# Kernel optimization log

Measured on AMD Instinct MI355X. Metric: run time of the kernel, lower is better.

The kernel has to match this reference:

```python
import jax, jax.numpy as jnp
import numpy as np
from jax import lax

B, T_ENC, T_DEC, F = 64, 1024, 256, 8
U = 256          # enc_units == dec_units
H, D = 8, 32     # num_heads * key_dim == U (residual constraint)
EPS = 1e-5


def layer_norm(x, g, b):
    m = jnp.mean(x, axis=-1, keepdims=True)
    v = jnp.mean(jnp.square(x - m), axis=-1, keepdims=True)
    return g * (x - m) / jnp.sqrt(v + EPS) + b


def lstm_scan(x, W, Urec, bias, h0, c0):
    # x: [B,T,F]; keras gate order i,f,g,o
    def step(carry, xt):
        h, c = carry
        z = xt @ W + h @ Urec + bias
        i, f, g, o = jnp.split(z, 4, axis=-1)
        c = jax.nn.sigmoid(f) * c + jax.nn.sigmoid(i) * jnp.tanh(g)
        h = jax.nn.sigmoid(o) * jnp.tanh(c)
        return (h, c), h
    (h, c), hs = lax.scan(step, (h0, c0), jnp.swapaxes(x, 0, 1))
    return jnp.swapaxes(hs, 0, 1), h, c


def mha(q_in, kv_in, Wq, bq, Wk, bk, Wv, bv, Wo, bo):
    Bq, Tq = q_in.shape[0], q_in.shape[1]
    Tk = kv_in.shape[1]
    q = (q_in @ Wq + bq).reshape(Bq, Tq, H, D).transpose(0, 2, 1, 3)
    k = (kv_in @ Wk + bk).reshape(Bq, Tk, H, D).transpose(0, 2, 1, 3)
    v = (kv_in @ Wv + bv).reshape(Bq, Tk, H, D).transpose(0, 2, 1, 3)
    scores = jnp.einsum('bhqd,bhkd->bhqk', q, k) * (D ** -0.5)
    w = jax.nn.softmax(scores, axis=-1)
    ctx = jnp.einsum('bhqk,bhkd->bhqd', w, v)
    ctx = ctx.transpose(0, 2, 1, 3).reshape(Bq, Tq, H * D)
    return ctx @ Wo + bo


def setup_inputs() -> dict:
    key = jax.random.key(0)
    ks = jax.random.split(key, 24)
    g = lambda k, s: (jax.random.normal(k, s, dtype=jnp.float32) * 0.05)
    return {
        'enc_in': jax.random.normal(ks[0], (B, T_ENC, F), dtype=jnp.float32),
        'dec_in': jax.random.normal(ks[1], (B, T_DEC, F), dtype=jnp.float32),
        'ln_enc_g': jnp.ones((F,), jnp.float32), 'ln_enc_b': jnp.zeros((F,), jnp.float32),
        'W_enc': g(ks[2], (F, 4 * U)), 'U_enc': g(ks[3], (U, 4 * U)), 'b_enc': jnp.zeros((4 * U,), jnp.float32),
        'W_dec': g(ks[4], (F, 4 * U)), 'U_dec': g(ks[5], (U, 4 * U)), 'b_dec': jnp.zeros((4 * U,), jnp.float32),
        'Wq': g(ks[6], (U, H * D)), 'bq': jnp.zeros((H * D,), jnp.float32),
        'Wk': g(ks[7], (U, H * D)), 'bk': jnp.zeros((H * D,), jnp.float32),
        'Wv': g(ks[8], (U, H * D)), 'bv': jnp.zeros((H * D,), jnp.float32),
        'Wo': g(ks[9], (H * D, H * D)), 'bo': jnp.zeros((H * D,), jnp.float32),
        'ln_post_g': jnp.ones((U,), jnp.float32), 'ln_post_b': jnp.zeros((U,), jnp.float32),
        'W_out': g(ks[10], (U, 1)), 'b_out': jnp.zeros((1,), jnp.float32),
    }


def reference(enc_in, dec_in, ln_enc_g, ln_enc_b, W_enc, U_enc, b_enc,
              W_dec, U_dec, b_dec, Wq, bq, Wk, bk, Wv, bv, Wo, bo,
              ln_post_g, ln_post_b, W_out, b_out):
    x = layer_norm(enc_in, ln_enc_g, ln_enc_b)
    h0 = jnp.zeros((enc_in.shape[0], U), enc_in.dtype)
    c0 = jnp.zeros((enc_in.shape[0], U), enc_in.dtype)
    enc_seq, h, c = lstm_scan(x, W_enc, U_enc, b_enc, h0, c0)
    dec_seq, _, _ = lstm_scan(dec_in, W_dec, U_dec, b_dec, h, c)
    ctx = mha(dec_seq, enc_seq, Wq, bq, Wk, bk, Wv, bv, Wo, bo)
    mix = layer_norm(dec_seq + ctx, ln_post_g, ln_post_b)
    return mix @ W_out + b_out
```

## Files before the change

kernel.cpp:

```cpp
#include <hip/hip_runtime.h>
#include <stdint.h>

#define NBATCH 64
#define TENC   1024
#define TDEC   256
#define FDIM   8
#define UDIM   256
#define GDIM   1024
#define NHEAD  8
#define DHEAD  32
#define LNEPS  1e-5f

#define KQ 33
#define KV 27
#define KL 6

typedef unsigned int   u32;
typedef unsigned short u16;

typedef _Float16 half2v __attribute__((ext_vector_type(2)));

__device__ __forceinline__ float bf2f_lo(u32 w) { return __uint_as_float(w << 16); }
__device__ __forceinline__ float bf2f_hi(u32 w) { return __uint_as_float(w & 0xFFFF0000u); }
__device__ __forceinline__ u16 f2bf(float f) {
  u32 u = __float_as_uint(f);
  u = (u + 0x7FFFu + ((u >> 16) & 1u)) >> 16;
  return (u16)u;
}
__device__ __forceinline__ u16 f2h_bits(float f) {
  _Float16 h = (_Float16)f;
  return __builtin_bit_cast(u16, h);
}
__device__ __forceinline__ float fdot2p(u32 wp, u32 hp, float acc) {
  return __builtin_amdgcn_fdot2(__builtin_bit_cast(half2v, wp),
                                __builtin_bit_cast(half2v, hp), acc, false);
}
__device__ __forceinline__ float sigf(float x) { return 1.0f / (1.0f + __expf(-x)); }
__device__ __forceinline__ float tanhf_fast(float x) {
  float ax = fabsf(x);
  float e  = __expf(2.0f * ax);
  float r  = 1.0f - 2.0f / (e + 1.0f);
  return copysignf(r, x);
}

__global__ __launch_bounds__(256)
void k_ln8(const float* __restrict__ x, const float* __restrict__ g,
           const float* __restrict__ bt, float* __restrict__ y, int rows) {
  int r = blockIdx.x * blockDim.x + threadIdx.x;
  if (r >= rows) return;
  const float* xp = x + (size_t)r * 8;
  float4 a = ((const float4*)xp)[0];
  float4 b4 = ((const float4*)xp)[1];
  float v[8] = {a.x, a.y, a.z, a.w, b4.x, b4.y, b4.z, b4.w};
  float m = 0.f;
#pragma unroll
  for (int i = 0; i < 8; ++i) m += v[i];
  m *= 0.125f;
  float var = 0.f;
#pragma unroll
  for (int i = 0; i < 8; ++i) { float d = v[i] - m; var += d * d; }
  var *= 0.125f;
  float rs = rsqrtf(var + LNEPS);
  float o[8];
#pragma unroll
  for (int i = 0; i < 8; ++i) o[i] = g[i] * (v[i] - m) * rs + bt[i];
  float* yp = y + (size_t)r * 8;
  ((float4*)yp)[0] = make_float4(o[0], o[1], o[2], o[3]);
  ((float4*)yp)[1] = make_float4(o[4], o[5], o[6], o[7]);
}

__global__ __launch_bounds__(256)
void k_packUW3(const float* __restrict__ U, const float* __restrict__ W,
               uint4* __restrict__ out) {
  int idx = blockIdx.x * 256 + threadIdx.x;
  if (idx >= KQ * GDIM) return;
  int q = idx >> 10, col = idx & 1023;
  uint4 o;
  u32* oc = (u32*)&o;
#pragma unroll
  for (int c = 0; c < 4; ++c) {
    int p = 4 * q + c;
    int r0 = 2 * p, r1 = 2 * p + 1;
    float f0 = (r0 < 256) ? U[(size_t)r0 * GDIM + col] : W[(size_t)(r0 - 256) * GDIM + col];
    float f1 = (r1 < 256) ? U[(size_t)r1 * GDIM + col] : W[(size_t)(r1 - 256) * GDIM + col];
    oc[c] = (u32)f2h_bits(f0) | ((u32)f2h_bits(f1) << 16);
  }
  out[idx] = o;
}

__global__
__attribute__((amdgpu_flat_work_group_size(512, 512), amdgpu_waves_per_eu(2, 2)))
void k_scan8(const float* __restrict__ xseq,
             const uint4* __restrict__ Wpk,
             const float* __restrict__ bias,
             const float* __restrict__ h0, const float* __restrict__ c0,
             float* __restrict__ seq_out,
             float* __restrict__ hT, float* __restrict__ cT, int T) {
  __shared__ __align__(16) uint4 wlA[KL * 512];
  __shared__ __align__(16) uint4 wlB[KL * 512];
  __shared__ __align__(16) u32   hpk[136];
  __shared__ float zl[1024];

  const int tid = threadIdx.x, b = blockIdx.x;
  const int colA = tid, colB = tid + 512;
  u16* hpk16 = (u16*)hpk;

  uint4 wvA[KV], wvB[KV];
#pragma unroll
  for (int q = 0; q < KV; ++q) {
    wvA[q] = Wpk[(q << 10) + colA];
    asm volatile("" : "+v"(wvA[q].x), "+v"(wvA[q].y), "+v"(wvA[q].z), "+v"(wvA[q].w));
    wvB[q] = Wpk[(q << 10) + colB];
    asm volatile("" : "+v"(wvB[q].x), "+v"(wvB[q].y), "+v"(wvB[q].z), "+v"(wvB[q].w));
  }
#pragma unroll
  for (int q = 0; q < KL; ++q) {
    wlA[q * 512 + tid] = Wpk[((KV + q) << 10) + colA];
    wlB[q * 512 + tid] = Wpk[((KV + q) << 10) + colB];
  }
  const float bA = bias[colA], bB = bias[colB];

  float c_reg = 0.f, h_last = 0.f;
  if (tid < 256) {
    float hv = h0 ? h0[b * 256 + tid] : 0.f;
    c_reg = c0 ? c0[b * 256 + tid] : 0.f;
    h_last = hv;
    hpk16[tid] = f2h_bits(hv);
  }
  if (tid >= 256 && tid < 264) {
    float xv = xseq[(size_t)(b * T) * 8 + (tid - 256)];
    hpk16[tid] = f2h_bits(xv);
  }
  __syncthreads();

  for (int t = 0; t < T; ++t) {
    float xn = 0.f;
    if (tid >= 256 && tid < 264) {
      int t2 = (t + 1 < T) ? (t + 1) : (T - 1);
      xn = xseq[(size_t)(b * T + t2) * 8 + (tid - 256)];
    }
    float a0 = bA, a1 = 0.f, a2 = 0.f, a3 = 0.f;
    float b0 = bB, b1 = 0.f, b2 = 0.f, b3 = 0.f;
    const uint4* hq4 = (const uint4*)hpk;
#pragma unroll
    for (int q = 0; q < KV; ++q) {
      uint4 hh = hq4[q];
      a0 = fdot2p(wvA[q].x, hh.x, a0); a1 = fdot2p(wvA[q].y, hh.y, a1);
      a2 = fdot2p(wvA[q].z, hh.z, a2); a3 = fdot2p(wvA[q].w, hh.w, a3);
      b0 = fdot2p(wvB[q].x, hh.x, b0); b1 = fdot2p(wvB[q].y, hh.y, b1);
      b2 = fdot2p(wvB[q].z, hh.z, b2); b3 = fdot2p(wvB[q].w, hh.w, b3);
    }
#pragma unroll
    for (int q = 0; q < KL; ++q) {
      uint4 hh = hq4[KV + q];
      uint4 wA = wlA[q * 512 + tid];
      uint4 wB = wlB[q * 512 + tid];
      a0 = fdot2p(wA.x, hh.x, a0); a1 = fdot2p(wA.y, hh.y, a1);
      a2 = fdot2p(wA.z, hh.z, a2); a3 = fdot2p(wA.w, hh.w, a3);
      b0 = fdot2p(wB.x, hh.x, b0); b1 = fdot2p(wB.y, hh.y, b1);
      b2 = fdot2p(wB.z, hh.z, b2); b3 = fdot2p(wB.w, hh.w, b3);
    }
    zl[colA] = (a0 + a1) + (a2 + a3);
    zl[colB] = (b0 + b1) + (b2 + b3);
    __syncthreads();

    if (tid < 256) {
      float zi = zl[tid], zf = zl[256 + tid], zg = zl[512 + tid], zo = zl[768 + tid];
      float ig = sigf(zi), fg = sigf(zf);
      float gg = tanhf_fast(zg), og = sigf(zo);
      c_reg = fg * c_reg + ig * gg;
      float h = og * tanhf_fast(c_reg);
      h_last = h;
      seq_out[(size_t)(b * T + t) * 256 + tid] = h;
      hpk16[tid] = f2h_bits(h);
    }
    if (tid >= 256 && tid < 264) hpk16[tid] = f2h_bits(xn);
    __syncthreads();
  }
  if (hT && tid < 256) {
    hT[b * 256 + tid] = h_last;
    cT[b * 256 + tid] = c_reg;
  }
}

template <int OMODE>
__global__ __launch_bounds__(256)
void k_gemm256(const float* __restrict__ A, const float* __restrict__ Bw,
               const float* __restrict__ bias, void* __restrict__ outp,
               int M, int Tdim) {
  __shared__ __align__(16) float As[16][68];
  __shared__ __align__(16) float Bs[16][68];
  const int tid = threadIdx.x;
  const int tx = tid & 15, ty = tid >> 4;
  const int bm = blockIdx.x * 64, bn = blockIdx.y * 64;
  const int ar = tid >> 2, ac = (tid & 3) << 2;
  const int br = tid >> 4, bc = (tid & 15) << 2;
  float acc[4][4] = {};
  for (int k0 = 0; k0 < 256; k0 += 16) {
    float4 av = *(const float4*)(A + (size_t)(bm + ar) * 256 + k0 + ac);
    As[ac + 0][ar] = av.x; As[ac + 1][ar] = av.y;
    As[ac + 2][ar] = av.z; As[ac + 3][ar] = av.w;
    float4 bv = *(const float4*)(Bw + (size_t)(k0 + br) * 256 + bn + bc);
    *(float4*)&Bs[br][bc] = bv;
    __syncthreads();
#pragma unroll
    for (int k = 0; k < 16; ++k) {
      float4 a4 = *(const float4*)&As[k][ty << 2];
      float4 b4 = *(const float4*)&Bs[k][tx << 2];
      float aa[4] = {a4.x, a4.y, a4.z, a4.w};
      float bb[4] = {b4.x, b4.y, b4.z, b4.w};
#pragma unroll
      for (int i = 0; i < 4; ++i)
#pragma unroll
        for (int jj = 0; jj < 4; ++jj)
          acc[i][jj] = fmaf(aa[i], bb[jj], acc[i][jj]);
    }
    __syncthreads();
  }
#pragma unroll
  for (int i = 0; i < 4; ++i) {
    int mm = bm + (ty << 2) + i;
#pragma unroll
    for (int jj = 0; jj < 4; ++jj) {
      int n = bn + (tx << 2) + jj;
      float v = acc[i][jj] + bias[n];
      if (OMODE == 0) {
        ((float*)outp)[(size_t)mm * 256 + n] = v;
      } else {
        int bb_ = mm / Tdim, t = mm % Tdim;
        int hh = n >> 5, dd = n & 31;
        size_t o = ((((size_t)bb_ * NHEAD + hh) * Tdim) + t) * 32 + dd;
        if (OMODE == 1) ((float*)outp)[o] = v;
        else            ((u16*)outp)[o]   = f2bf(v);
      }
    }
  }
}

__global__ __launch_bounds__(256)
void k_attn(const float* __restrict__ Q, const u16* __restrict__ Kb,
            const u16* __restrict__ Vb, float* __restrict__ ctx) {
  const int bh = blockIdx.x;
  const int b = bh >> 3, h = bh & 7;
  const int tid = threadIdx.x;
  __shared__ __align__(16) float Kl[64][36];
  __shared__ __align__(16) float Vl[64][36];
  float q[32];
  {
    const float* qp = Q + ((size_t)bh * TDEC + tid) * 32;
#pragma unroll
    for (int i = 0; i < 8; ++i) {
      float4 v = ((const float4*)qp)[i];
      q[i * 4 + 0] = v.x * 0.17677669529663687f;
      q[i * 4 + 1] = v.y * 0.17677669529663687f;
      q[i * 4 + 2] = v.z * 0.17677669529663687f;
      q[i * 4 + 3] = v.w * 0.17677669529663687f;
    }
  }
  float mrun = -3.0e38f, lrun = 0.f;
  float acc[32];
#pragma unroll
  for (int i = 0; i < 32; ++i) acc[i] = 0.f;
  const int lr = tid >> 2, lc = (tid & 3) << 3;
  for (int kt = 0; kt < TENC; kt += 64) {
    {
      uint4 kw = *(const uint4*)(Kb + ((size_t)bh * TENC + kt + lr) * 32 + lc);
      Kl[lr][lc + 0] = bf2f_lo(kw.x); Kl[lr][lc + 1] = bf2f_hi(kw.x);
      Kl[lr][lc + 2] = bf2f_lo(kw.y); Kl[lr][lc + 3] = bf2f_hi(kw.y);
      Kl[lr][lc + 4] = bf2f_lo(kw.z); Kl[lr][lc + 5] = bf2f_hi(kw.z);
      Kl[lr][lc + 6] = bf2f_lo(kw.w); Kl[lr][lc + 7] = bf2f_hi(kw.w);
      uint4 vw = *(const uint4*)(Vb + ((size_t)bh * TENC + kt + lr) * 32 + lc);
      Vl[lr][lc + 0] = bf2f_lo(vw.x); Vl[lr][lc + 1] = bf2f_hi(vw.x);
      Vl[lr][lc + 2] = bf2f_lo(vw.y); Vl[lr][lc + 3] = bf2f_hi(vw.y);
      Vl[lr][lc + 4] = bf2f_lo(vw.z); Vl[lr][lc + 5] = bf2f_hi(vw.z);
      Vl[lr][lc + 6] = bf2f_lo(vw.w); Vl[lr][lc + 7] = bf2f_hi(vw.w);
    }
    __syncthreads();
#pragma unroll
    for (int cch = 0; cch < 8; ++cch) {
      float s8[8];
#pragma unroll
      for (int i = 0; i < 8; ++i) {
        const float4* kr = (const float4*)&Kl[cch * 8 + i][0];
        float ss = 0.f;
#pragma unroll
        for (int d4 = 0; d4 < 8; ++d4) {
          float4 kv = kr[d4];
          ss = fmaf(q[d4 * 4 + 0], kv.x, ss);
          ss = fmaf(q[d4 * 4 + 1], kv.y, ss);
          ss = fmaf(q[d4 * 4 + 2], kv.z, ss);
          ss = fmaf(q[d4 * 4 + 3], kv.w, ss);
        }
        s8[i] = ss;
      }
      float mnew = mrun;
#pragma unroll
      for (int i = 0; i < 8; ++i) mnew = fmaxf(mnew, s8[i]);
      float sc = __expf(mrun - mnew);
      mrun = mnew;
      lrun *= sc;
#pragma unroll
      for (int d = 0; d < 32; ++d) acc[d] *= sc;
#pragma unroll
      for (int i = 0; i < 8; ++i) {
        float p = __expf(s8[i] - mnew);
        lrun += p;
        const float4* vr = (const float4*)&Vl[cch * 8 + i][0];
#pragma unroll
        for (int d4 = 0; d4 < 8; ++d4) {
          float4 vv = vr[d4];
          acc[d4 * 4 + 0] = fmaf(p, vv.x, acc[d4 * 4 + 0]);
          acc[d4 * 4 + 1] = fmaf(p, vv.y, acc[d4 * 4 + 1]);
          acc[d4 * 4 + 2] = fmaf(p, vv.z, acc[d4 * 4 + 2]);
          acc[d4 * 4 + 3] = fmaf(p, vv.w, acc[d4 * 4 + 3]);
        }
      }
    }
    __syncthreads();
  }
  float inv = 1.0f / lrun;
  float* op = ctx + ((size_t)(b * TDEC + tid) * 256 + h * 32);
#pragma unroll
  for (int i = 0; i < 8; ++i) {
    ((float4*)op)[i] = make_float4(acc[i * 4 + 0] * inv, acc[i * 4 + 1] * inv,
                                   acc[i * 4 + 2] * inv, acc[i * 4 + 3] * inv);
  }
}

__global__ __launch_bounds__(256)
void k_final(const float* __restrict__ dec_seq, const float* __restrict__ ctxo,
             const float* __restrict__ g, const float* __restrict__ bb,
             const float* __restrict__ Wout, const float* __restrict__ bout,
             float* __restrict__ out) {
  const int wv = threadIdx.x >> 6, lane = threadIdx.x & 63;
  const int row = blockIdx.x * 4 + wv;
  const size_t base = (size_t)row * 256 + lane * 4;
  float4 dv = *(const float4*)(dec_seq + base);
  float4 cv = *(const float4*)(ctxo + base);
  float v[4] = {dv.x + cv.x, dv.y + cv.y, dv.z + cv.z, dv.w + cv.w};
  float s = v[0] + v[1] + v[2] + v[3];
#pragma unroll
  for (int off = 32; off >= 1; off >>= 1) s += __shfl_xor(s, off, 64);
  float m = s * (1.0f / 256.0f);
  float d2 = 0.f;
#pragma unroll
  for (int i = 0; i < 4; ++i) { float d = v[i] - m; d2 += d * d; }
#pragma unroll
  for (int off = 32; off >= 1; off >>= 1) d2 += __shfl_xor(d2, off, 64);
  float rs = rsqrtf(d2 * (1.0f / 256.0f) + LNEPS);
  float4 g4 = *(const float4*)(g + lane * 4);
  float4 b4 = *(const float4*)(bb + lane * 4);
  float4 w4 = *(const float4*)(Wout + lane * 4);
  float mix0 = g4.x * (v[0] - m) * rs + b4.x;
  float mix1 = g4.y * (v[1] - m) * rs + b4.y;
  float mix2 = g4.z * (v[2] - m) * rs + b4.z;
  float mix3 = g4.w * (v[3] - m) * rs + b4.w;
  float p = mix0 * w4.x + mix1 * w4.y + mix2 * w4.z + mix3 * w4.w;
#pragma unroll
  for (int off = 32; off >= 1; off >>= 1) p += __shfl_xor(p, off, 64);
  if (lane == 0) out[row] = p + bout[0];
}

extern "C" void kernel_launch(void* const* d_in, const int* in_sizes, int n_in,
                              void* d_out, int out_size, void* d_ws, size_t ws_size,
                              hipStream_t stream) {
  const float* enc_in   = (const float*)d_in[0];
  const float* dec_in   = (const float*)d_in[1];
  const float* ln_enc_g = (const float*)d_in[2];
  const float* ln_enc_b = (const float*)d_in[3];
  const float* W_enc    = (const float*)d_in[4];
  const float* U_enc    = (const float*)d_in[5];
  const float* b_enc    = (const float*)d_in[6];
  const float* W_dec    = (const float*)d_in[7];
  const float* U_dec    = (const float*)d_in[8];
  const float* b_dec    = (const float*)d_in[9];
  const float* Wq = (const float*)d_in[10]; const float* bq = (const float*)d_in[11];
  const float* Wk = (const float*)d_in[12]; const float* bk = (const float*)d_in[13];
  const float* Wv = (const float*)d_in[14]; const float* bv = (const float*)d_in[15];
  const float* Wo = (const float*)d_in[16]; const float* bo = (const float*)d_in[17];
  const float* ln_post_g = (const float*)d_in[18];
  const float* ln_post_b = (const float*)d_in[19];
  const float* W_out     = (const float*)d_in[20];
  const float* b_out     = (const float*)d_in[21];

  char* ws = (char*)d_ws;
  size_t off = 0;
  auto alloc = [&](size_t bytes) -> void* {
    void* p = ws + off;
    off += (bytes + 255) & ~(size_t)255;
    return p;
  };
  float* xln     = (float*)alloc((size_t)NBATCH * TENC * 8 * 4);
  uint4* upkE    = (uint4*)alloc((size_t)KQ * GDIM * 16);
  uint4* upkD    = (uint4*)alloc((size_t)KQ * GDIM * 16);
  float* enc_seq = (float*)alloc((size_t)NBATCH * TENC * 256 * 4);
  float* dec_seq = (float*)alloc((size_t)NBATCH * TDEC * 256 * 4);
  float* hfin    = (float*)alloc((size_t)NBATCH * 256 * 4);
  float* cfin    = (float*)alloc((size_t)NBATCH * 256 * 4);
  float* Qp      = (float*)alloc((size_t)NBATCH * NHEAD * TDEC * 32 * 4);
  u16*   Kb      = (u16*)  alloc((size_t)NBATCH * NHEAD * TENC * 32 * 2);
  u16*   Vb      = (u16*)  alloc((size_t)NBATCH * NHEAD * TENC * 32 * 2);
  float* ctx     = (float*)alloc((size_t)NBATCH * TDEC * 256 * 4);
  float* ctxo    = (float*)alloc((size_t)NBATCH * TDEC * 256 * 4);

  k_ln8<<<dim3(256), dim3(256), 0, stream>>>(enc_in, ln_enc_g, ln_enc_b, xln,
                                             NBATCH * TENC);
  k_packUW3<<<dim3(132), dim3(256), 0, stream>>>(U_enc, W_enc, upkE);
  k_packUW3<<<dim3(132), dim3(256), 0, stream>>>(U_dec, W_dec, upkD);
  k_scan8<<<dim3(NBATCH), dim3(512), 0, stream>>>(
      xln, upkE, b_enc, nullptr, nullptr, enc_seq, hfin, cfin, TENC);
  k_scan8<<<dim3(NBATCH), dim3(512), 0, stream>>>(
      dec_in, upkD, b_dec, hfin, cfin, dec_seq, nullptr, nullptr, TDEC);
  k_gemm256<1><<<dim3(256, 4), dim3(256), 0, stream>>>(dec_seq, Wq, bq, Qp, NBATCH * TDEC, TDEC);
  k_gemm256<2><<<dim3(1024, 4), dim3(256), 0, stream>>>(enc_seq, Wk, bk, Kb, NBATCH * TENC, TENC);
  k_gemm256<2><<<dim3(1024, 4), dim3(256), 0, stream>>>(enc_seq, Wv, bv, Vb, NBATCH * TENC, TENC);
  k_attn<<<dim3(NBATCH * NHEAD), dim3(256), 0, stream>>>(Qp, Kb, Vb, ctx);
  k_gemm256<0><<<dim3(256, 4), dim3(256), 0, stream>>>(ctx, Wo, bo, ctxo, NBATCH * TDEC, 0x7fffffff);
  k_final<<<dim3(NBATCH * TDEC / 4), dim3(256), 0, stream>>>(
      dec_seq, ctxo, ln_post_g, ln_post_b, W_out, b_out, (float*)d_out);
}
```

Before: 3.561 ms.

## Split LSTM recurrent weights across registers, LDS and streamed global loads

The recurrent scan kernel now keeps only 9 of 33 weight quads per column in registers and 9 in LDS, and streams the remaining 15 from global/L2 on every timestep. Previously 27 quads sat in registers and 6 in LDS. The hidden-state buffer is also double-buffered by timestep parity. The intent is to relieve register pressure, since the kernel is pinned to 2 waves per EU, but every one of the serial steps now pays L2 load latency.

```diff
diff --git a/kernel.cpp b/kernel.cpp
--- a/kernel.cpp
+++ b/kernel.cpp
@@ -11,9 +11,10 @@
 #define DHEAD  32
 #define LNEPS  1e-5f
 
-#define KQ 33
-#define KV 27
-#define KL 6
+#define KQ   33
+#define KPIN 9
+#define KLDS 9
+#define KSTR 15
 
 typedef unsigned int   u32;
 typedef unsigned short u16;
@@ -88,80 +89,99 @@
   out[idx] = o;
 }
 
+#define DOTP(w4, hh)                                              \
+  do {                                                            \
+    a0 = fdot2p((w4).x, (hh).x, a0);                              \
+    a1 = fdot2p((w4).y, (hh).y, a1);                              \
+    a2 = fdot2p((w4).z, (hh).z, a2);                              \
+    a3 = fdot2p((w4).w, (hh).w, a3);                              \
+  } while (0)
+#define DOTQ(w4, hh)                                              \
+  do {                                                            \
+    d0 = fdot2p((w4).x, (hh).x, d0);                              \
+    d1 = fdot2p((w4).y, (hh).y, d1);                              \
+    d2 = fdot2p((w4).z, (hh).z, d2);                              \
+    d3 = fdot2p((w4).w, (hh).w, d3);                              \
+  } while (0)
+
 __global__
 __attribute__((amdgpu_flat_work_group_size(512, 512), amdgpu_waves_per_eu(2, 2)))
-void k_scan8(const float* __restrict__ xseq,
-             const uint4* __restrict__ Wpk,
-             const float* __restrict__ bias,
-             const float* __restrict__ h0, const float* __restrict__ c0,
-             float* __restrict__ seq_out,
-             float* __restrict__ hT, float* __restrict__ cT, int T) {
-  __shared__ __align__(16) uint4 wlA[KL * 512];
-  __shared__ __align__(16) uint4 wlB[KL * 512];
-  __shared__ __align__(16) u32   hpk[136];
+void k_scan11(const float* __restrict__ xseq,
+              const uint4* __restrict__ Wpk,
+              const float* __restrict__ bias,
+              const float* __restrict__ h0, const float* __restrict__ c0,
+              float* __restrict__ seq_out,
+              float* __restrict__ hT, float* __restrict__ cT, int T) {
+  __shared__ __align__(16) uint4 wl[2 * KLDS][512];
   __shared__ float zl[1024];
+  __shared__ __align__(16) u32 hbuf[2][136];
 
   const int tid = threadIdx.x, b = blockIdx.x;
-  const int colA = tid, colB = tid + 512;
-  u16* hpk16 = (u16*)hpk;
-
-  uint4 wvA[KV], wvB[KV];
-#pragma unroll
-  for (int q = 0; q < KV; ++q) {
-    wvA[q] = Wpk[(q << 10) + colA];
-    asm volatile("" : "+v"(wvA[q].x), "+v"(wvA[q].y), "+v"(wvA[q].z), "+v"(wvA[q].w));
-    wvB[q] = Wpk[(q << 10) + colB];
-    asm volatile("" : "+v"(wvB[q].x), "+v"(wvB[q].y), "+v"(wvB[q].z), "+v"(wvB[q].w));
-  }
-#pragma unroll
-  for (int q = 0; q < KL; ++q) {
-    wlA[q * 512 + tid] = Wpk[((KV + q) << 10) + colA];
-    wlB[q * 512 + tid] = Wpk[((KV + q) << 10) + colB];
-  }
-  const float bA = bias[colA], bB = bias[colB];
+  const int cA = tid, cB = tid + 512;
+
+  uint4 wpA[KPIN], wpB[KPIN];
+#pragma unroll
+  for (int i = 0; i < KPIN; ++i) {
+    wpA[i] = Wpk[(i << 10) + cA];
+    asm("" : "+v"(wpA[i].x), "+v"(wpA[i].y), "+v"(wpA[i].z), "+v"(wpA[i].w));
+    wpB[i] = Wpk[(i << 10) + cB];
+    asm("" : "+v"(wpB[i].x), "+v"(wpB[i].y), "+v"(wpB[i].z), "+v"(wpB[i].w));
+  }
+#pragma unroll
+  for (int i = 0; i < KLDS; ++i) {
+    wl[i][tid]        = Wpk[((KPIN + i) << 10) + cA];
+    wl[KLDS + i][tid] = Wpk[((KPIN + i) << 10) + cB];
+  }
+  const uint4* wstr = Wpk + ((KPIN + KLDS) << 10);
+
+  const float bA = bias[cA], bB = bias[cB];
 
   float c_reg = 0.f, h_last = 0.f;
   if (tid < 256) {
-    float hv = h0 ? h0[b * 256 + tid] : 0.f;
-    c_reg = c0 ? c0[b * 256 + tid] : 0.f;
-    h_last = hv;
-    hpk16[tid] = f2h_bits(hv);
+    c_reg  = c0 ? c0[b * 256 + tid] : 0.f;
+    h_last = h0 ? h0[b * 256 + tid] : 0.f;
+    ((u16*)hbuf[0])[tid] = f2h_bits(h_last);
   }
   if (tid >= 256 && tid < 264) {
     float xv = xseq[(size_t)(b * T) * 8 + (tid - 256)];
-    hpk16[tid] = f2h_bits(xv);
+    ((u16*)hbuf[0])[tid] = f2h_bits(xv);
   }
   __syncthreads();
 
   for (int t = 0; t < T; ++t) {
+    const int pr = t & 1, nx = pr ^ 1;
     float xn = 0.f;
     if (tid >= 256 && tid < 264) {
       int t2 = (t + 1 < T) ? (t + 1) : (T - 1);
       xn = xseq[(size_t)(b * T + t2) * 8 + (tid - 256)];
     }
     float a0 = bA, a1 = 0.f, a2 = 0.f, a3 = 0.f;
-    float b0 = bB, b1 = 0.f, b2 = 0.f, b3 = 0.f;
-    const uint4* hq4 = (const uint4*)hpk;
-#pragma unroll
-    for (int q = 0; q < KV; ++q) {
+    float d0 = bB, d1 = 0.f, d2 = 0.f, d3 = 0.f;
+    const uint4* hq4 = (const uint4*)hbuf[pr];
+#pragma unroll
+    for (int q = 0; q < KPIN; ++q) {
       uint4 hh = hq4[q];
-      a0 = fdot2p(wvA[q].x, hh.x, a0); a1 = fdot2p(wvA[q].y, hh.y, a1);
-      a2 = fdot2p(wvA[q].z, hh.z, a2); a3 = fdot2p(wvA[q].w, hh.w, a3);
-      b0 = fdot2p(wvB[q].x, hh.x, b0); b1 = fdot2p(wvB[q].y, hh.y, b1);
-      b2 = fdot2p(wvB[q].z, hh.z, b2); b3 = fdot2p(wvB[q].w, hh.w, b3);
-    }
-#pragma unroll
-    for (int q = 0; q < KL; ++q) {
-      uint4 hh = hq4[KV + q];
-      uint4 wA = wlA[q * 512 + tid];
-      uint4 wB = wlB[q * 512 + tid];
-      a0 = fdot2p(wA.x, hh.x, a0); a1 = fdot2p(wA.y, hh.y, a1);
-      a2 = fdot2p(wA.z, hh.z, a2); a3 = fdot2p(wA.w, hh.w, a3);
-      b0 = fdot2p(wB.x, hh.x, b0); b1 = fdot2p(wB.y, hh.y, b1);
-      b2 = fdot2p(wB.z, hh.z, b2); b3 = fdot2p(wB.w, hh.w, b3);
-    }
-    zl[colA] = (a0 + a1) + (a2 + a3);
-    zl[colB] = (b0 + b1) + (b2 + b3);
+      DOTP(wpA[q], hh);
+      DOTQ(wpB[q], hh);
+    }
+#pragma unroll
+    for (int q = 0; q < KLDS; ++q) {
+      uint4 hh = hq4[KPIN + q];
+      uint4 wA = wl[q][tid];
+      uint4 wB = wl[KLDS + q][tid];
+      DOTP(wA, hh);
+      DOTQ(wB, hh);
+    }
+#pragma unroll
+    for (int q = 0; q < KSTR; ++q) {
+      uint4 hh = hq4[KPIN + KLDS + q];
+      uint4 wA = wstr[(q << 10) + cA];
+      uint4 wB = wstr[(q << 10) + cB];
+      DOTP(wA, hh);
+      DOTQ(wB, hh);
+    }
+    zl[cA] = (a0 + a1) + (a2 + a3);
+    zl[cB] = (d0 + d1) + (d2 + d3);
     __syncthreads();
 
     if (tid < 256) {
@@ -172,9 +192,9 @@
       float h = og * tanhf_fast(c_reg);
       h_last = h;
       seq_out[(size_t)(b * T + t) * 256 + tid] = h;
-      hpk16[tid] = f2h_bits(h);
-    }
-    if (tid >= 256 && tid < 264) hpk16[tid] = f2h_bits(xn);
+      ((u16*)hbuf[nx])[tid] = f2h_bits(h);
+    }
+    if (tid >= 256 && tid < 264) ((u16*)hbuf[nx])[tid] = f2h_bits(xn);
     __syncthreads();
   }
   if (hT && tid < 256) {
@@ -407,9 +427,9 @@
                                              NBATCH * TENC);
   k_packUW3<<<dim3(132), dim3(256), 0, stream>>>(U_enc, W_enc, upkE);
   k_packUW3<<<dim3(132), dim3(256), 0, stream>>>(U_dec, W_dec, upkD);
-  k_scan8<<<dim3(NBATCH), dim3(512), 0, stream>>>(
+  k_scan11<<<dim3(NBATCH), dim3(512), 0, stream>>>(
       xln, upkE, b_enc, nullptr, nullptr, enc_seq, hfin, cfin, TENC);
-  k_scan8<<<dim3(NBATCH), dim3(512), 0, stream>>>(
+  k_scan11<<<dim3(NBATCH), dim3(512), 0, stream>>>(
       dec_in, upkD, b_dec, hfin, cfin, dec_seq, nullptr, nullptr, TDEC);
   k_gemm256<1><<<dim3(256, 4), dim3(256), 0, stream>>>(dec_seq, Wq, bq, Qp, NBATCH * TDEC, TDEC);
   k_gemm256<2><<<dim3(1024, 4), dim3(256), 0, stream>>>(enc_seq, Wk, bk, Kb, NBATCH * TENC, TENC);
```

Result: faster. 3.453 ms (-3.0%).
